# Kernel tuning notes

Measured on AMD Instinct MI355X. Metric: run time of the kernel, lower is better.

## Reference

```python
import jax, jax.numpy as jnp
import numpy as np

IN_C = 128
OUT_C = 128
HEADS = 8
HEAD_DIM = OUT_C // HEADS
N_NODES = 4096
N_EDGES = 131072


def setup_inputs() -> dict:
    key = jax.random.key(0)
    ks = jax.random.split(key, 10)
    s_in = 1.0 / np.sqrt(IN_C)
    s_out = 1.0 / np.sqrt(OUT_C)
    return {
        "x": jax.random.normal(ks[0], (N_NODES, IN_C), dtype=jnp.float32),
        "edge_index": jax.random.randint(ks[1], (2, N_EDGES), 0, N_NODES, dtype=jnp.int64),
        "Wq": jax.random.uniform(ks[2], (IN_C, OUT_C), jnp.float32, -s_in, s_in),
        "bq": jnp.zeros((OUT_C,), jnp.float32),
        "Wk": jax.random.uniform(ks[3], (IN_C, OUT_C), jnp.float32, -s_in, s_in),
        "bk": jnp.zeros((OUT_C,), jnp.float32),
        "Wv": jax.random.uniform(ks[4], (IN_C, OUT_C), jnp.float32, -s_in, s_in),
        "bv": jnp.zeros((OUT_C,), jnp.float32),
        "Wo": jax.random.uniform(ks[5], (OUT_C, OUT_C), jnp.float32, -s_out, s_out),
        "bo": jnp.zeros((OUT_C,), jnp.float32),
    }


def reference(x, edge_index, Wq, bq, Wk, bk, Wv, bv, Wo, bo):
    n = x.shape[0]
    Q = (x @ Wq + bq).reshape(n, HEADS, HEAD_DIM)
    K = (x @ Wk + bk).reshape(n, HEADS, HEAD_DIM)
    V = (x @ Wv + bv).reshape(n, HEADS, HEAD_DIM)
    # dense scores [n, m, h], matching the original module's einsum
    scores = jnp.einsum('nhd,mhd->nmh', Q, K) / np.sqrt(HEAD_DIM).astype(np.float32)
    ei = jnp.clip(edge_index, 0, n - 1)
    mask = jnp.zeros((n, n), dtype=bool).at[ei[0], ei[1]].set(True)
    scores = jnp.where(mask[:, :, None], scores, -jnp.inf)
    attention = jax.nn.softmax(scores, axis=1)
    # rows (along m) that were all -inf give NaN -> replace with 1/n, as in torch
    attention = jnp.nan_to_num(attention, nan=1.0 / n)
    out = jnp.einsum('nmh,mhd->nhd', attention, V).reshape(n, OUT_C)
    return out @ Wo + bo
```

## Files before the change

### kernel.cpp

```cpp
#include <hip/hip_runtime.h>
#include <math.h>

#define NN 4096
#define NE 131072
#define C 128
#define NH 8
#define HD 16
#define UCAP 64

__device__ __forceinline__ float dot16(const float* __restrict__ q, const float* __restrict__ kp) {
    const float4* k4 = reinterpret_cast<const float4*>(kp);
    const float4 k0 = k4[0], k1 = k4[1], k2 = k4[2], k3 = k4[3];
    return q[0]*k0.x + q[1]*k0.y + q[2]*k0.z + q[3]*k0.w
         + q[4]*k1.x + q[5]*k1.y + q[6]*k1.z + q[7]*k1.w
         + q[8]*k2.x + q[9]*k2.y + q[10]*k2.z + q[11]*k2.w
         + q[12]*k3.x + q[13]*k3.y + q[14]*k3.z + q[15]*k3.w;
}

__global__ __launch_bounds__(512) void qkv_kernel(
    const float* __restrict__ x,
    const float* __restrict__ Wq, const float* __restrict__ bq,
    const float* __restrict__ Wk, const float* __restrict__ bk,
    const float* __restrict__ Wv, const float* __restrict__ bv,
    float* __restrict__ Q, float* __restrict__ K, float* __restrict__ V,
    float4* __restrict__ mask_clear)
{
    const int tid = threadIdx.x;
    mask_clear[blockIdx.x * 512 + tid] = make_float4(0.f, 0.f, 0.f, 0.f);

    __shared__ float xs[16][C];
    const int n0 = blockIdx.x * 16;
    reinterpret_cast<float4*>(&xs[0][0])[tid] =
        reinterpret_cast<const float4*>(x + n0 * C)[tid];
    __syncthreads();

    const int c = tid & 127;
    const int q = tid >> 7;
    float aq[4], ak[4], av[4];
    #pragma unroll
    for (int j = 0; j < 4; j++) { aq[j] = 0.f; ak[j] = 0.f; av[j] = 0.f; }

    #pragma unroll 4
    for (int k = 0; k < C; k++) {
        const float wq = Wq[k * C + c];
        const float wk = Wk[k * C + c];
        const float wv = Wv[k * C + c];
        #pragma unroll
        for (int j = 0; j < 4; j++) {
            const float xv = xs[q + 4 * j][k];
            aq[j] = fmaf(xv, wq, aq[j]);
            ak[j] = fmaf(xv, wk, ak[j]);
            av[j] = fmaf(xv, wv, av[j]);
        }
    }
    const float bqv = bq[c], bkv = bk[c], bvv = bv[c];
    #pragma unroll
    for (int j = 0; j < 4; j++) {
        const int n = n0 + q + 4 * j;
        Q[n * C + c] = aq[j] + bqv;
        K[n * C + c] = ak[j] + bkv;
        V[n * C + c] = av[j] + bvv;
    }
}

__global__ __launch_bounds__(256) void mask_kernel(
    const int* __restrict__ ei, unsigned int* __restrict__ mask)
{
    const int e = blockIdx.x * 256 + threadIdx.x;
    int src = ei[e];
    int dst = ei[NE + e];
    src = src < 0 ? 0 : (src > NN - 1 ? NN - 1 : src);
    dst = dst < 0 ? 0 : (dst > NN - 1 ? NN - 1 : dst);
    atomicOr(&mask[(src << 7) + (dst >> 5)], 1u << (dst & 31));
}

__global__ __launch_bounds__(256, 2) void attn_proj_kernel(
    const float* __restrict__ Q, const float* __restrict__ K,
    const float* __restrict__ V, const unsigned int* __restrict__ mask,
    const float* __restrict__ Wo, const float* __restrict__ bo,
    float* __restrict__ out)
{
    __shared__ unsigned short lst[4][UCAP];
    __shared__ float row[4][C];

    const int tid = threadIdx.x;
    const int w = tid >> 6;
    const int lane = tid & 63;
    const int base = blockIdx.x * 4;
    const int nl = w;
    const int n = base + nl;
    const int h = lane & 7;
    const int sub = lane >> 3;

    {
        const unsigned int* rowp = mask + (n << 7);
        unsigned int b0 = rowp[lane * 2];
        unsigned int b1 = rowp[lane * 2 + 1];
        const int myc = __popc(b0) + __popc(b1);
        int incl = myc;
        #pragma unroll
        for (int d = 1; d < 64; d <<= 1) {
            const int t = __shfl_up(incl, d, 64);
            if (lane >= d) incl += t;
        }
        const int deg = __shfl(incl, 63, 64);
        int o = incl - myc;
        const int idbase = lane * 64;
        while (b0) {
            const int b = __ffs(b0) - 1; b0 &= b0 - 1;
            if (o < UCAP) lst[nl][o] = (unsigned short)(idbase + b);
            o++;
        }
        while (b1) {
            const int b = __ffs(b1) - 1; b1 &= b1 - 1;
            if (o < UCAP) lst[nl][o] = (unsigned short)(idbase + 32 + b);
            o++;
        }
        asm volatile("s_waitcnt lgkmcnt(0)" ::: "memory");
        const int dg = min(deg, UCAP);

        if (dg == 0) {
            for (int d = lane; d < C; d += 64) {
                float s2 = 0.f;
                for (int m = 0; m < NN; m++) s2 += V[m * C + d];
                row[nl][d] = s2 * (1.f / (float)NN);
            }
        } else {
            float qh[16];
            {
                const float4* qp = reinterpret_cast<const float4*>(Q + n * C + h * HD);
                const float4 q0 = qp[0], q1 = qp[1], q2 = qp[2], q3 = qp[3];
                qh[0]=q0.x; qh[1]=q0.y; qh[2]=q0.z; qh[3]=q0.w;
                qh[4]=q1.x; qh[5]=q1.y; qh[6]=q1.z; qh[7]=q1.w;
                qh[8]=q2.x; qh[9]=q2.y; qh[10]=q2.z; qh[11]=q2.w;
                qh[12]=q3.x; qh[13]=q3.y; qh[14]=q3.z; qh[15]=q3.w;
            }
            int id[8];
            #pragma unroll
            for (int j = 0; j < 8; j++) {
                const int i = sub + 8 * j;
                id[j] = (i < dg) ? (int)lst[nl][i] : -1;
            }

            float acc[16];
            #pragma unroll
            for (int d = 0; d < 16; d++) acc[d] = 0.f;
            float s[8];

            float4 va[4][4];
            #pragma unroll
            for (int j = 0; j < 4; j++) {
                const int idx = id[j] >= 0 ? id[j] : 0;
                s[j] = (id[j] >= 0) ? dot16(qh, K + idx * C + h * HD) * 0.25f : -INFINITY;
                const float4* vp = reinterpret_cast<const float4*>(V + idx * C + h * HD);
                va[j][0] = vp[0]; va[j][1] = vp[1]; va[j][2] = vp[2]; va[j][3] = vp[3];
            }
            const float mA = fmaxf(fmaxf(s[0], s[1]), fmaxf(s[2], s[3]));
            float ssum = 0.f;
            #pragma unroll
            for (int j = 0; j < 4; j++) {
                const float p = (id[j] >= 0) ? __expf(s[j] - mA) : 0.f;
                ssum += p;
                acc[0]  = fmaf(p, va[j][0].x, acc[0]);  acc[1]  = fmaf(p, va[j][0].y, acc[1]);
                acc[2]  = fmaf(p, va[j][0].z, acc[2]);  acc[3]  = fmaf(p, va[j][0].w, acc[3]);
                acc[4]  = fmaf(p, va[j][1].x, acc[4]);  acc[5]  = fmaf(p, va[j][1].y, acc[5]);
                acc[6]  = fmaf(p, va[j][1].z, acc[6]);  acc[7]  = fmaf(p, va[j][1].w, acc[7]);
                acc[8]  = fmaf(p, va[j][2].x, acc[8]);  acc[9]  = fmaf(p, va[j][2].y, acc[9]);
                acc[10] = fmaf(p, va[j][2].z, acc[10]); acc[11] = fmaf(p, va[j][2].w, acc[11]);
                acc[12] = fmaf(p, va[j][3].x, acc[12]); acc[13] = fmaf(p, va[j][3].y, acc[13]);
                acc[14] = fmaf(p, va[j][3].z, acc[14]); acc[15] = fmaf(p, va[j][3].w, acc[15]);
            }

            float ml = mA;
            if (dg > 32) {
                float4 vb[4][4];
                #pragma unroll
                for (int j = 4; j < 8; j++) {
                    const int idx = id[j] >= 0 ? id[j] : 0;
                    s[j] = (id[j] >= 0) ? dot16(qh, K + idx * C + h * HD) * 0.25f : -INFINITY;
                    const float4* vp = reinterpret_cast<const float4*>(V + idx * C + h * HD);
                    vb[j-4][0] = vp[0]; vb[j-4][1] = vp[1]; vb[j-4][2] = vp[2]; vb[j-4][3] = vp[3];
                }
                const float mB = fmaxf(fmaxf(s[4], s[5]), fmaxf(s[6], s[7]));
                ml = fmaxf(mA, mB);
                const float fA = (ml == -INFINITY) ? 0.f : __expf(mA - ml);
                ssum *= fA;
                #pragma unroll
                for (int d = 0; d < 16; d++) acc[d] *= fA;
                #pragma unroll
                for (int j = 4; j < 8; j++) {
                    const float p = (id[j] >= 0) ? __expf(s[j] - ml) : 0.f;
                    ssum += p;
                    acc[0]  = fmaf(p, vb[j-4][0].x, acc[0]);  acc[1]  = fmaf(p, vb[j-4][0].y, acc[1]);
                    acc[2]  = fmaf(p, vb[j-4][0].z, acc[2]);  acc[3]  = fmaf(p, vb[j-4][0].w, acc[3]);
                    acc[4]  = fmaf(p, vb[j-4][1].x, acc[4]);  acc[5]  = fmaf(p, vb[j-4][1].y, acc[5]);
                    acc[6]  = fmaf(p, vb[j-4][1].z, acc[6]);  acc[7]  = fmaf(p, vb[j-4][1].w, acc[7]);
                    acc[8]  = fmaf(p, vb[j-4][2].x, acc[8]);  acc[9]  = fmaf(p, vb[j-4][2].y, acc[9]);
                    acc[10] = fmaf(p, vb[j-4][2].z, acc[10]); acc[11] = fmaf(p, vb[j-4][2].w, acc[11]);
                    acc[12] = fmaf(p, vb[j-4][3].x, acc[12]); acc[13] = fmaf(p, vb[j-4][3].y, acc[13]);
                    acc[14] = fmaf(p, vb[j-4][3].z, acc[14]); acc[15] = fmaf(p, vb[j-4][3].w, acc[15]);
                }
            }

            float M = ml;
            #pragma unroll
            for (int o2 = 8; o2 < 64; o2 <<= 1) M = fmaxf(M, __shfl_xor(M, o2, 64));
            const float f = (ml == -INFINITY) ? 0.f : __expf(ml - M);
            ssum *= f;
            #pragma unroll
            for (int d = 0; d < 16; d++) acc[d] *= f;
            #pragma unroll
            for (int o2 = 8; o2 < 64; o2 <<= 1) ssum += __shfl_xor(ssum, o2, 64);
            #pragma unroll
            for (int o2 = 8; o2 < 64; o2 <<= 1) {
                #pragma unroll
                for (int d = 0; d < 16; d++)
                    acc[d] += __shfl_xor(acc[d], o2, 64);
            }
            const float inv = 1.f / ssum;
            if (sub == 0) {
                float4* rp = reinterpret_cast<float4*>(&row[nl][h * HD]);
                rp[0] = make_float4(acc[0]*inv,  acc[1]*inv,  acc[2]*inv,  acc[3]*inv);
                rp[1] = make_float4(acc[4]*inv,  acc[5]*inv,  acc[6]*inv,  acc[7]*inv);
                rp[2] = make_float4(acc[8]*inv,  acc[9]*inv,  acc[10]*inv, acc[11]*inv);
                rp[3] = make_float4(acc[12]*inv, acc[13]*inv, acc[14]*inv, acc[15]*inv);
            }
        }
    }
    __syncthreads();

    const int c = tid & 127;
    const int r = tid >> 7;
    float a0 = 0.f, a1 = 0.f;
    #pragma unroll 4
    for (int k = 0; k < C; k++) {
        const float wo = Wo[k * C + c];
        a0 = fmaf(row[r][k],     wo, a0);
        a1 = fmaf(row[r + 2][k], wo, a1);
    }
    const float bov = bo[c];
    out[(base + r) * C + c]     = a0 + bov;
    out[(base + r + 2) * C + c] = a1 + bov;
}

extern "C" void kernel_launch(void* const* d_in, const int* in_sizes, int n_in,
                              void* d_out, int out_size, void* d_ws, size_t ws_size,
                              hipStream_t stream)
{
    const float* x  = (const float*)d_in[0];
    const int*   ei = (const int*)d_in[1];
    const float* Wq = (const float*)d_in[2];
    const float* bq = (const float*)d_in[3];
    const float* Wk = (const float*)d_in[4];
    const float* bk = (const float*)d_in[5];
    const float* Wv = (const float*)d_in[6];
    const float* bv = (const float*)d_in[7];
    const float* Wo = (const float*)d_in[8];
    const float* bo = (const float*)d_in[9];
    float* out = (float*)d_out;

    char* ws = (char*)d_ws;
    const size_t MB2 = 1u << 21;
    float*        Q    = (float*)(ws);
    float*        K    = (float*)(ws + MB2);
    float*        V    = (float*)(ws + 2 * MB2);
    unsigned int* mask = (unsigned int*)(ws + 3 * MB2);

    qkv_kernel<<<NN / 16, 512, 0, stream>>>(x, Wq, bq, Wk, bk, Wv, bv, Q, K, V,
                                            (float4*)mask);
    mask_kernel<<<NE / 256, 256, 0, stream>>>(ei, mask);
    attn_proj_kernel<<<NN / 4, 256, 0, stream>>>(Q, K, V, mask, Wo, bo, out);
}
```

Before: 50.20 us.

## Split attention into two-pass softmax and raise occupancy bound to six

```diff
diff --git a/kernel.cpp b/kernel.cpp
--- a/kernel.cpp
+++ b/kernel.cpp
@@ -74,7 +74,7 @@
     atomicOr(&mask[(src << 7) + (dst >> 5)], 1u << (dst & 31));
 }
 
-__global__ __launch_bounds__(256, 2) void attn_proj_kernel(
+__global__ __launch_bounds__(256, 6) void attn_proj_kernel(
     const float* __restrict__ Q, const float* __restrict__ K,
     const float* __restrict__ V, const unsigned int* __restrict__ mask,
     const float* __restrict__ Wo, const float* __restrict__ bo,
@@ -135,95 +135,97 @@
                 qh[8]=q2.x; qh[9]=q2.y; qh[10]=q2.z; qh[11]=q2.w;
                 qh[12]=q3.x; qh[13]=q3.y; qh[14]=q3.z; qh[15]=q3.w;
             }
-            int id[8];
-            #pragma unroll
-            for (int j = 0; j < 8; j++) {
+
+            float s[8];
+
+            #pragma unroll
+            for (int j = 0; j < 4; j++) {
                 const int i = sub + 8 * j;
-                id[j] = (i < dg) ? (int)lst[nl][i] : -1;
-            }
+                const int idx = (i < dg) ? (int)lst[nl][i] : 0;
+                s[j] = (i < dg) ? dot16(qh, K + idx * C + h * HD) * 0.25f : -INFINITY;
+            }
+            float ml = fmaxf(fmaxf(s[0], s[1]), fmaxf(s[2], s[3]));
+            if (dg > 32) {
+                #pragma unroll
+                for (int j = 4; j < 8; j++) {
+                    const int i = sub + 8 * j;
+                    const int idx = (i < dg) ? (int)lst[nl][i] : 0;
+                    s[j] = (i < dg) ? dot16(qh, K + idx * C + h * HD) * 0.25f : -INFINITY;
+                }
+                ml = fmaxf(ml, fmaxf(fmaxf(s[4], s[5]), fmaxf(s[6], s[7])));
+            }
+
+            float M = ml;
+            #pragma unroll
+            for (int o2 = 8; o2 < 64; o2 <<= 1) M = fmaxf(M, __shfl_xor(M, o2, 64));
+
+            float ssum = 0.f;
+            #pragma unroll
+            for (int j = 0; j < 4; j++) {
+                s[j] = (sub + 8 * j < dg) ? __expf(s[j] - M) : 0.f;
+                ssum += s[j];
+            }
+            if (dg > 32) {
+                #pragma unroll
+                for (int j = 4; j < 8; j++) {
+                    s[j] = (sub + 8 * j < dg) ? __expf(s[j] - M) : 0.f;
+                    ssum += s[j];
+                }
+            }
+            #pragma unroll
+            for (int o2 = 8; o2 < 64; o2 <<= 1) ssum += __shfl_xor(ssum, o2, 64);
+            const float inv = 1.f / ssum;
 
             float acc[16];
             #pragma unroll
             for (int d = 0; d < 16; d++) acc[d] = 0.f;
-            float s[8];
-
-            float4 va[4][4];
             #pragma unroll
             for (int j = 0; j < 4; j++) {
-                const int idx = id[j] >= 0 ? id[j] : 0;
-                s[j] = (id[j] >= 0) ? dot16(qh, K + idx * C + h * HD) * 0.25f : -INFINITY;
+                const int i = sub + 8 * j;
+                const int idx = (i < dg) ? (int)lst[nl][i] : 0;
+                const float p = s[j] * inv;
                 const float4* vp = reinterpret_cast<const float4*>(V + idx * C + h * HD);
-                va[j][0] = vp[0]; va[j][1] = vp[1]; va[j][2] = vp[2]; va[j][3] = vp[3];
-            }
-            const float mA = fmaxf(fmaxf(s[0], s[1]), fmaxf(s[2], s[3]));
-            float ssum = 0.f;
-            #pragma unroll
-            for (int j = 0; j < 4; j++) {
-                const float p = (id[j] >= 0) ? __expf(s[j] - mA) : 0.f;
-                ssum += p;
-                acc[0]  = fmaf(p, va[j][0].x, acc[0]);  acc[1]  = fmaf(p, va[j][0].y, acc[1]);
-                acc[2]  = fmaf(p, va[j][0].z, acc[2]);  acc[3]  = fmaf(p, va[j][0].w, acc[3]);
-                acc[4]  = fmaf(p, va[j][1].x, acc[4]);  acc[5]  = fmaf(p, va[j][1].y, acc[5]);
-                acc[6]  = fmaf(p, va[j][1].z, acc[6]);  acc[7]  = fmaf(p, va[j][1].w, acc[7]);
-                acc[8]  = fmaf(p, va[j][2].x, acc[8]);  acc[9]  = fmaf(p, va[j][2].y, acc[9]);
-                acc[10] = fmaf(p, va[j][2].z, acc[10]); acc[11] = fmaf(p, va[j][2].w, acc[11]);
-                acc[12] = fmaf(p, va[j][3].x, acc[12]); acc[13] = fmaf(p, va[j][3].y, acc[13]);
-                acc[14] = fmaf(p, va[j][3].z, acc[14]); acc[15] = fmaf(p, va[j][3].w, acc[15]);
-            }
-
-            float ml = mA;
+                const float4 v0 = vp[0], v1 = vp[1], v2 = vp[2], v3 = vp[3];
+                acc[0]  = fmaf(p, v0.x, acc[0]);  acc[1]  = fmaf(p, v0.y, acc[1]);
+                acc[2]  = fmaf(p, v0.z, acc[2]);  acc[3]  = fmaf(p, v0.w, acc[3]);
+                acc[4]  = fmaf(p, v1.x, acc[4]);  acc[5]  = fmaf(p, v1.y, acc[5]);
+                acc[6]  = fmaf(p, v1.z, acc[6]);  acc[7]  = fmaf(p, v1.w, acc[7]);
+                acc[8]  = fmaf(p, v2.x, acc[8]);  acc[9]  = fmaf(p, v2.y, acc[9]);
+                acc[10] = fmaf(p, v2.z, acc[10]); acc[11] = fmaf(p, v2.w, acc[11]);
+                acc[12] = fmaf(p, v3.x, acc[12]); acc[13] = fmaf(p, v3.y, acc[13]);
+                acc[14] = fmaf(p, v3.z, acc[14]); acc[15] = fmaf(p, v3.w, acc[15]);
+            }
             if (dg > 32) {
-                float4 vb[4][4];
                 #pragma unroll
                 for (int j = 4; j < 8; j++) {
-                    const int idx = id[j] >= 0 ? id[j] : 0;
-                    s[j] = (id[j] >= 0) ? dot16(qh, K + idx * C + h * HD) * 0.25f : -INFINITY;
+                    const int i = sub + 8 * j;
+                    const int idx = (i < dg) ? (int)lst[nl][i] : 0;
+                    const float p = s[j] * inv;
                     const float4* vp = reinterpret_cast<const float4*>(V + idx * C + h * HD);
-                    vb[j-4][0] = vp[0]; vb[j-4][1] = vp[1]; vb[j-4][2] = vp[2]; vb[j-4][3] = vp[3];
+                    const float4 v0 = vp[0], v1 = vp[1], v2 = vp[2], v3 = vp[3];
+                    acc[0]  = fmaf(p, v0.x, acc[0]);  acc[1]  = fmaf(p, v0.y, acc[1]);
+                    acc[2]  = fmaf(p, v0.z, acc[2]);  acc[3]  = fmaf(p, v0.w, acc[3]);
+                    acc[4]  = fmaf(p, v1.x, acc[4]);  acc[5]  = fmaf(p, v1.y, acc[5]);
+                    acc[6]  = fmaf(p, v1.z, acc[6]);  acc[7]  = fmaf(p, v1.w, acc[7]);
+                    acc[8]  = fmaf(p, v2.x, acc[8]);  acc[9]  = fmaf(p, v2.y, acc[9]);
+                    acc[10] = fmaf(p, v2.z, acc[10]); acc[11] = fmaf(p, v2.w, acc[11]);
+                    acc[12] = fmaf(p, v3.x, acc[12]); acc[13] = fmaf(p, v3.y, acc[13]);
+                    acc[14] = fmaf(p, v3.z, acc[14]); acc[15] = fmaf(p, v3.w, acc[15]);
                 }
-                const float mB = fmaxf(fmaxf(s[4], s[5]), fmaxf(s[6], s[7]));
-                ml = fmaxf(mA, mB);
-                const float fA = (ml == -INFINITY) ? 0.f : __expf(mA - ml);
-                ssum *= fA;
-                #pragma unroll
-                for (int d = 0; d < 16; d++) acc[d] *= fA;
-                #pragma unroll
-                for (int j = 4; j < 8; j++) {
-                    const float p = (id[j] >= 0) ? __expf(s[j] - ml) : 0.f;
-                    ssum += p;
-                    acc[0]  = fmaf(p, vb[j-4][0].x, acc[0]);  acc[1]  = fmaf(p, vb[j-4][0].y, acc[1]);
-                    acc[2]  = fmaf(p, vb[j-4][0].z, acc[2]);  acc[3]  = fmaf(p, vb[j-4][0].w, acc[3]);
-                    acc[4]  = fmaf(p, vb[j-4][1].x, acc[4]);  acc[5]  = fmaf(p, vb[j-4][1].y, acc[5]);
-                    acc[6]  = fmaf(p, vb[j-4][1].z, acc[6]);  acc[7]  = fmaf(p, vb[j-4][1].w, acc[7]);
-                    acc[8]  = fmaf(p, vb[j-4][2].x, acc[8]);  acc[9]  = fmaf(p, vb[j-4][2].y, acc[9]);
-                    acc[10] = fmaf(p, vb[j-4][2].z, acc[10]); acc[11] = fmaf(p, vb[j-4][2].w, acc[11]);
-                    acc[12] = fmaf(p, vb[j-4][3].x, acc[12]); acc[13] = fmaf(p, vb[j-4][3].y, acc[13]);
-                    acc[14] = fmaf(p, vb[j-4][3].z, acc[14]); acc[15] = fmaf(p, vb[j-4][3].w, acc[15]);
-                }
-            }
-
-            float M = ml;
-            #pragma unroll
-            for (int o2 = 8; o2 < 64; o2 <<= 1) M = fmaxf(M, __shfl_xor(M, o2, 64));
-            const float f = (ml == -INFINITY) ? 0.f : __expf(ml - M);
-            ssum *= f;
-            #pragma unroll
-            for (int d = 0; d < 16; d++) acc[d] *= f;
-            #pragma unroll
-            for (int o2 = 8; o2 < 64; o2 <<= 1) ssum += __shfl_xor(ssum, o2, 64);
+            }
+
             #pragma unroll
             for (int o2 = 8; o2 < 64; o2 <<= 1) {
                 #pragma unroll
                 for (int d = 0; d < 16; d++)
                     acc[d] += __shfl_xor(acc[d], o2, 64);
             }
-            const float inv = 1.f / ssum;
             if (sub == 0) {
                 float4* rp = reinterpret_cast<float4*>(&row[nl][h * HD]);
-                rp[0] = make_float4(acc[0]*inv,  acc[1]*inv,  acc[2]*inv,  acc[3]*inv);
-                rp[1] = make_float4(acc[4]*inv,  acc[5]*inv,  acc[6]*inv,  acc[7]*inv);
-                rp[2] = make_float4(acc[8]*inv,  acc[9]*inv,  acc[10]*inv, acc[11]*inv);
-                rp[3] = make_float4(acc[12]*inv, acc[13]*inv, acc[14]*inv, acc[15]*inv);
+                rp[0] = make_float4(acc[0],  acc[1],  acc[2],  acc[3]);
+                rp[1] = make_float4(acc[4],  acc[5],  acc[6],  acc[7]);
+                rp[2] = make_float4(acc[8],  acc[9],  acc[10], acc[11]);
+                rp[3] = make_float4(acc[12], acc[13], acc[14], acc[15]);
             }
         }
     }
```

New measurement: 51.38 us. +2.3%, slower.
